# Kernel optimization log

Measured on AMD Instinct MI355X. Metric: run time of the kernel, lower is better.

## Reference

```python
import jax, jax.numpy as jnp
import numpy as np

B, S, P, V, D = 8, 32, 8, 8000, 128
CONC = 5.0  # concentrator_factor
EPS = 1e-8  # torch cosine_similarity eps


def setup_inputs() -> dict:
    key = jax.random.key(0)
    ks = jax.random.split(key, 8)
    concepts = jax.random.randint(ks[0], (B, S, P), 0, V)
    concepts_length = jax.random.randint(ks[1], (B, S), 0, P + 1)
    seg_len = jax.random.randint(ks[2], (B,), 1, S + 1)
    embed_w = jax.random.normal(ks[3], (V, D), jnp.float32)
    embed_kb_w = jax.random.normal(ks[4], (V, D), jnp.float32)
    edge_matrix = jax.random.uniform(ks[5], (V, V), jnp.float32)
    affectiveness = jax.random.uniform(ks[6], (V,), jnp.float32)
    lam = jnp.full((V,), 0.5, jnp.float32)  # _lambda init to GAW
    return dict(concepts=concepts, concepts_length=concepts_length, seg_len=seg_len,
                embed_w=embed_w, embed_kb_w=embed_kb_w, edge_matrix=edge_matrix,
                affectiveness=affectiveness, lam=lam)


def reference(concepts, concepts_length, seg_len, embed_w, embed_kb_w,
              edge_matrix, affectiveness, lam):
    f32 = embed_w.dtype
    # init_params: normalize edge_matrix rows by their range
    rng = edge_matrix.max(axis=1) - edge_matrix.min(axis=1)  # [V]
    em = edge_matrix / (rng + (rng == 0).astype(f32))[:, None]

    ce = embed_w[concepts]  # [B,S,P,D]
    # ragged mean over P (empty -> zeros, matching empty_tensor)
    pmask = (jnp.arange(P)[None, None, :] < concepts_length[:, :, None]).astype(f32)  # [B,S,P]
    denom = jnp.maximum(concepts_length, 1).astype(f32)[:, :, None]  # [B,S,1]
    mean_j = (ce * pmask[..., None]).sum(axis=2) / denom  # [B,S,D]
    # mean over valid segments j < seg_len
    smask = (jnp.arange(S)[None, :] < seg_len[:, None]).astype(f32)  # [B,S]
    context = (mean_j * smask[..., None]).sum(axis=1) / seg_len.astype(f32)[:, None]  # [B,D]

    # abs cosine similarity vs KB embedding table
    cn = context / jnp.maximum(jnp.linalg.norm(context, axis=1, keepdims=True), EPS)
    kn = embed_kb_w / jnp.maximum(jnp.linalg.norm(embed_kb_w, axis=1, keepdims=True), EPS)
    cos = jnp.abs(cn @ kn.T)  # [B,V]

    eg = em[concepts]  # [B,S,P,V] irregular row gather
    rel = eg * cos[:, None, None, :]
    aff = (eg > 0).astype(f32) * affectiveness
    w = lam * rel + (1.0 - lam) * aff  # [B,S,P,V]
    attn = jax.nn.softmax(w * CONC, axis=3)
    ce2 = attn @ embed_kb_w  # [B,S,P,D]

    # ragged mean over P again, zero out segments j >= seg_len (padded output)
    out = (ce2 * pmask[..., None]).sum(axis=2) / denom  # [B,S,D]
    out = out * smask[..., None]
    return out
```

## Files before the change

kernel.cpp:

```cpp
#include <hip/hip_runtime.h>
#include <cmath>

#define NB 8
#define NS 32
#define NP 8
#define NV 8000
#define ND 128
#define CONC 5.0f
#define EPS 1e-8f

#define TROWS 8
#define USPLIT 25
#define URANGE 320
#define UCHUNK 64
#define NCHUNK (URANGE / UCHUNK)
#define MAXSLOTS (NB * NS * NP)

#define WS_COUNTER 0
#define WS_META_C  16
#define WS_META_O  2064
#define WS_IRNG    4112
#define WS_GMAX    6160
#define WS_SCALE   8208
#define WS_CN      10256
#define WS_COS     11280
#define WS_MEANJ   75280

__global__ void k_mean(const int* __restrict__ concepts,
                       const int* __restrict__ concepts_length,
                       const float* __restrict__ embed_w,
                       float* __restrict__ mean_j) {
    const int bs = blockIdx.x;
    const int d = threadIdx.x;
    const int len = concepts_length[bs];
    float sum = 0.0f;
    for (int p = 0; p < len; ++p) {
        const int c = concepts[bs * NP + p];
        sum += embed_w[(size_t)c * ND + d];
    }
    mean_j[(size_t)bs * ND + d] = sum / (float)(len > 0 ? len : 1);
}

__global__ void k_ctx2(const int* __restrict__ seg_len,
                       const float* __restrict__ mean_j,
                       float* __restrict__ cn) {
    const int b = blockIdx.x;
    const int d = threadIdx.x;
    const int sl = seg_len[b];
    float acc = 0.0f;
    for (int s = 0; s < sl; ++s) acc += mean_j[(size_t)(b * NS + s) * ND + d];
    acc /= (float)sl;
    float ss = acc * acc;
    #pragma unroll
    for (int m = 1; m < 64; m <<= 1) ss += __shfl_xor(ss, m);
    __shared__ float sred[2];
    if ((d & 63) == 0) sred[d >> 6] = ss;
    __syncthreads();
    const float tot = sred[0] + sred[1];
    cn[b * ND + d] = acc / fmaxf(sqrtf(tot), EPS);
}

__global__ __launch_bounds__(256) void k_cos(const float* __restrict__ kb,
                                             const float* __restrict__ cn,
                                             float* __restrict__ cos_bv) {
    __shared__ float s_cn[NB * ND];
    const int t = threadIdx.x;
    for (int i = t; i < NB * ND; i += 256) s_cn[i] = cn[i];
    __syncthreads();

    const int v = blockIdx.x * 8 + (t >> 5);
    const int l = t & 31;
    const float4 kv = *reinterpret_cast<const float4*>(kb + (size_t)v * ND + (l << 2));
    float ss = kv.x * kv.x + kv.y * kv.y + kv.z * kv.z + kv.w * kv.w;
    #pragma unroll
    for (int m = 1; m < 32; m <<= 1) ss += __shfl_xor(ss, m);
    const float inv = 1.0f / fmaxf(sqrtf(ss), EPS);
    #pragma unroll
    for (int b = 0; b < NB; ++b) {
        const float4 cv = *reinterpret_cast<const float4*>(&s_cn[b * ND + (l << 2)]);
        float dot = kv.x * cv.x + kv.y * cv.y + kv.z * cv.z + kv.w * cv.w;
        #pragma unroll
        for (int m = 1; m < 32; m <<= 1) dot += __shfl_xor(dot, m);
        if (l == 0) cos_bv[b * NV + v] = fabsf(dot * inv);
    }
}

__global__ __launch_bounds__(256) void k_A(
        const int* __restrict__ concepts,
        const int* __restrict__ concepts_length,
        const int* __restrict__ seg_len,
        const float* __restrict__ edge,
        const float* __restrict__ aff,
        const float* __restrict__ lam,
        const float* __restrict__ cos_bv,
        int* __restrict__ counter,
        int* __restrict__ meta_c, int* __restrict__ meta_out,
        float* __restrict__ f_irng, float* __restrict__ f_gmax,
        float* __restrict__ f_scale) {
    const int idx = blockIdx.x;
    const int b = idx >> 8;
    const int s = (idx >> 3) & 31;
    const int p = idx & 7;
    if (s >= seg_len[b]) return;
    const int len = concepts_length[b * NS + s];
    if (p >= len) return;
    const int c = concepts[idx];

    const int t = threadIdx.x;
    const float* __restrict__ erow = edge + (size_t)c * NV;
    float4 ev[8];
    float lmax = -INFINITY, lmin = INFINITY;
    #pragma unroll
    for (int k = 0; k < 8; ++k) {
        const int f = t + (k << 8);
        if (f < 2000) {
            const float4 e = *reinterpret_cast<const float4*>(erow + (f << 2));
            ev[k] = e;
            lmax = fmaxf(lmax, fmaxf(fmaxf(e.x, e.y), fmaxf(e.z, e.w)));
            lmin = fminf(lmin, fminf(fminf(e.x, e.y), fminf(e.z, e.w)));
        }
    }
    #pragma unroll
    for (int m = 1; m < 64; m <<= 1) {
        lmax = fmaxf(lmax, __shfl_xor(lmax, m));
        lmin = fminf(lmin, __shfl_xor(lmin, m));
    }
    __shared__ float s_min[4], s_max[4], s_wm[4], s_sum[4];
    if ((t & 63) == 0) { s_min[t >> 6] = lmin; s_max[t >> 6] = lmax; }
    __syncthreads();
    const float rmin = fminf(fminf(s_min[0], s_min[1]), fminf(s_min[2], s_min[3]));
    const float rmax = fmaxf(fmaxf(s_max[0], s_max[1]), fmaxf(s_max[2], s_max[3]));
    const float rng = rmax - rmin;
    const float inv_rng = 1.0f / (rng + (rng == 0.0f ? 1.0f : 0.0f));

    const float* __restrict__ cosb = cos_bv + b * NV;
    float wmax = -INFINITY;
    #pragma unroll
    for (int k = 0; k < 8; ++k) {
        const int f = t + (k << 8);
        if (f < 2000) {
            const int u = f << 2;
            const float4 l4 = *reinterpret_cast<const float4*>(lam + u);
            const float4 a4 = *reinterpret_cast<const float4*>(aff + u);
            const float4 c4 = *reinterpret_cast<const float4*>(cosb + u);
            float4 e = ev[k];
            e.x *= inv_rng; e.y *= inv_rng; e.z *= inv_rng; e.w *= inv_rng;
            float4 w;
            w.x = (l4.x * e.x * c4.x + (1.0f - l4.x) * ((e.x > 0.0f) ? 1.0f : 0.0f) * a4.x) * CONC;
            w.y = (l4.y * e.y * c4.y + (1.0f - l4.y) * ((e.y > 0.0f) ? 1.0f : 0.0f) * a4.y) * CONC;
            w.z = (l4.z * e.z * c4.z + (1.0f - l4.z) * ((e.z > 0.0f) ? 1.0f : 0.0f) * a4.z) * CONC;
            w.w = (l4.w * e.w * c4.w + (1.0f - l4.w) * ((e.w > 0.0f) ? 1.0f : 0.0f) * a4.w) * CONC;
            ev[k] = w;
            wmax = fmaxf(wmax, fmaxf(fmaxf(w.x, w.y), fmaxf(w.z, w.w)));
        } else {
            ev[k] = make_float4(-INFINITY, -INFINITY, -INFINITY, -INFINITY);
        }
    }
    #pragma unroll
    for (int m = 1; m < 64; m <<= 1) wmax = fmaxf(wmax, __shfl_xor(wmax, m));
    if ((t & 63) == 0) s_wm[t >> 6] = wmax;
    __syncthreads();
    const float gmax = fmaxf(fmaxf(s_wm[0], s_wm[1]), fmaxf(s_wm[2], s_wm[3]));

    float lsum = 0.0f;
    #pragma unroll
    for (int k = 0; k < 8; ++k) {
        lsum += __expf(ev[k].x - gmax);
        lsum += __expf(ev[k].y - gmax);
        lsum += __expf(ev[k].z - gmax);
        lsum += __expf(ev[k].w - gmax);
    }
    #pragma unroll
    for (int m = 1; m < 64; m <<= 1) lsum += __shfl_xor(lsum, m);
    if ((t & 63) == 0) s_sum[t >> 6] = lsum;
    __syncthreads();
    if (t == 0) {
        const float total = s_sum[0] + s_sum[1] + s_sum[2] + s_sum[3];
        const int slot = atomicAdd(counter, 1);
        meta_c[slot] = c;
        meta_out[slot] = b * NS + s;
        f_irng[slot] = inv_rng;
        f_gmax[slot] = gmax;
        f_scale[slot] = 1.0f / (total * (float)len);
    }
}

__global__ __launch_bounds__(256) void k_B(
        const float* __restrict__ edge,
        const float* __restrict__ aff,
        const float* __restrict__ lam,
        const float* __restrict__ kb,
        const float* __restrict__ cos_bv,
        const int* __restrict__ counter,
        const int* __restrict__ meta_c, const int* __restrict__ meta_out,
        const float* __restrict__ f_irng, const float* __restrict__ f_gmax,
        const float* __restrict__ f_scale,
        float* __restrict__ out) {
    const int count = counter[0];
    const int tile = blockIdx.x;
    if (tile * TROWS >= count) return;

    const int t = threadIdx.x;
    const int ug = t & 7;
    const int l = t >> 3;

    __shared__ int s_c[TROWS], s_o[TROWS], s_b[TROWS];
    __shared__ float s_irng[TROWS], s_gmax[TROWS], s_scale[TROWS];
    __shared__ __align__(16) float s_p[UCHUNK * TROWS];

    if (t < TROWS) {
        const int slot = tile * TROWS + t;
        if (slot < count) {
            const int c = meta_c[slot];
            const int o = meta_out[slot];
            s_c[t] = c; s_o[t] = o; s_b[t] = o >> 5;
            s_irng[t] = f_irng[slot];
            s_gmax[t] = f_gmax[slot];
            s_scale[t] = f_scale[slot];
        } else {
            s_c[t] = -1; s_o[t] = 0; s_b[t] = 0;
            s_irng[t] = 0.0f; s_gmax[t] = 0.0f; s_scale[t] = 0.0f;
        }
    }
    __syncthreads();

    const int u0 = blockIdx.y * URANGE;

    float4 acc[TROWS];
    #pragma unroll
    for (int j = 0; j < TROWS; ++j) acc[j] = make_float4(0.f, 0.f, 0.f, 0.f);

    for (int ch = 0; ch < NCHUNK; ++ch) {
        const int uc = u0 + ch * UCHUNK;

        #pragma unroll
        for (int rep = 0; rep < 2; ++rep) {
            const int ii = t + (rep << 8);
            const int slot = ii & 7;
            const int uu = ii >> 3;
            const int cc = s_c[slot];
            float pv = 0.0f;
            if (cc >= 0) {
                const int u = uc + uu;
                const float e = edge[(size_t)cc * NV + u] * s_irng[slot];
                const float lm = lam[u];
                const float w = (lm * e * cos_bv[(size_t)s_b[slot] * NV + u]
                                 + (1.0f - lm) * ((e > 0.0f) ? 1.0f : 0.0f) * aff[u]) * CONC;
                pv = __expf(w - s_gmax[slot]);
            }
            s_p[ii] = pv;
        }
        __syncthreads();

        #pragma unroll
        for (int r = 0; r < 8; ++r) {
            const int uu = ug + (r << 3);
            const float4 kv = *reinterpret_cast<const float4*>(
                kb + (size_t)(uc + uu) * ND + (l << 2));
            const float4 p0 = *reinterpret_cast<const float4*>(&s_p[uu * TROWS]);
            const float4 p1 = *reinterpret_cast<const float4*>(&s_p[uu * TROWS + 4]);
            acc[0].x = fmaf(p0.x, kv.x, acc[0].x); acc[0].y = fmaf(p0.x, kv.y, acc[0].y);
            acc[0].z = fmaf(p0.x, kv.z, acc[0].z); acc[0].w = fmaf(p0.x, kv.w, acc[0].w);
            acc[1].x = fmaf(p0.y, kv.x, acc[1].x); acc[1].y = fmaf(p0.y, kv.y, acc[1].y);
            acc[1].z = fmaf(p0.y, kv.z, acc[1].z); acc[1].w = fmaf(p0.y, kv.w, acc[1].w);
            acc[2].x = fmaf(p0.z, kv.x, acc[2].x); acc[2].y = fmaf(p0.z, kv.y, acc[2].y);
            acc[2].z = fmaf(p0.z, kv.z, acc[2].z); acc[2].w = fmaf(p0.z, kv.w, acc[2].w);
            acc[3].x = fmaf(p0.w, kv.x, acc[3].x); acc[3].y = fmaf(p0.w, kv.y, acc[3].y);
            acc[3].z = fmaf(p0.w, kv.z, acc[3].z); acc[3].w = fmaf(p0.w, kv.w, acc[3].w);
            acc[4].x = fmaf(p1.x, kv.x, acc[4].x); acc[4].y = fmaf(p1.x, kv.y, acc[4].y);
            acc[4].z = fmaf(p1.x, kv.z, acc[4].z); acc[4].w = fmaf(p1.x, kv.w, acc[4].w);
            acc[5].x = fmaf(p1.y, kv.x, acc[5].x); acc[5].y = fmaf(p1.y, kv.y, acc[5].y);
            acc[5].z = fmaf(p1.y, kv.z, acc[5].z); acc[5].w = fmaf(p1.y, kv.w, acc[5].w);
            acc[6].x = fmaf(p1.z, kv.x, acc[6].x); acc[6].y = fmaf(p1.z, kv.y, acc[6].y);
            acc[6].z = fmaf(p1.z, kv.z, acc[6].z); acc[6].w = fmaf(p1.z, kv.w, acc[6].w);
            acc[7].x = fmaf(p1.w, kv.x, acc[7].x); acc[7].y = fmaf(p1.w, kv.y, acc[7].y);
            acc[7].z = fmaf(p1.w, kv.z, acc[7].z); acc[7].w = fmaf(p1.w, kv.w, acc[7].w);
        }
        __syncthreads();
    }

    float4 res = make_float4(0.f, 0.f, 0.f, 0.f);
    #pragma unroll
    for (int j = 0; j < TROWS; ++j) {
        float4 a = acc[j];
        #pragma unroll
        for (int m = 1; m <= 4; m <<= 1) {
            a.x += __shfl_xor(a.x, m);
            a.y += __shfl_xor(a.y, m);
            a.z += __shfl_xor(a.z, m);
            a.w += __shfl_xor(a.w, m);
        }
        if (ug == j) res = a;
    }

    const int myslot = tile * TROWS + ug;
    if (myslot < count && s_c[ug] >= 0) {
        const float sc = s_scale[ug];
        float* o = out + (size_t)s_o[ug] * ND + (l << 2);
        atomicAdd(o + 0, res.x * sc);
        atomicAdd(o + 1, res.y * sc);
        atomicAdd(o + 2, res.z * sc);
        atomicAdd(o + 3, res.w * sc);
    }
}

extern "C" void kernel_launch(void* const* d_in, const int* in_sizes, int n_in,
                              void* d_out, int out_size, void* d_ws, size_t ws_size,
                              hipStream_t stream) {
    const int*   concepts        = (const int*)d_in[0];
    const int*   concepts_length = (const int*)d_in[1];
    const int*   seg_len         = (const int*)d_in[2];
    const float* embed_w         = (const float*)d_in[3];
    const float* embed_kb_w      = (const float*)d_in[4];
    const float* edge_matrix     = (const float*)d_in[5];
    const float* affectiveness   = (const float*)d_in[6];
    const float* lam             = (const float*)d_in[7];
    float* out = (float*)d_out;

    float* wsf = (float*)d_ws;
    int*   wsi = (int*)d_ws;
    int*   counter  = wsi + WS_COUNTER;
    int*   meta_c   = wsi + WS_META_C;
    int*   meta_out = wsi + WS_META_O;
    float* f_irng   = wsf + WS_IRNG;
    float* f_gmax   = wsf + WS_GMAX;
    float* f_scale  = wsf + WS_SCALE;
    float* cn       = wsf + WS_CN;
    float* cos_bv   = wsf + WS_COS;
    float* mean_j   = wsf + WS_MEANJ;

    hipMemsetAsync(out, 0, (size_t)out_size * sizeof(float), stream);
    hipMemsetAsync(counter, 0, 64, stream);

    k_mean<<<NB * NS, ND, 0, stream>>>(concepts, concepts_length, embed_w, mean_j);
    k_ctx2<<<NB, ND, 0, stream>>>(seg_len, mean_j, cn);
    k_cos<<<NV / 8, 256, 0, stream>>>(embed_kb_w, cn, cos_bv);
    k_A<<<MAXSLOTS, 256, 0, stream>>>(concepts, concepts_length, seg_len,
                                      edge_matrix, affectiveness, lam, cos_bv,
                                      counter, meta_c, meta_out,
                                      f_irng, f_gmax, f_scale);
    dim3 gB(MAXSLOTS / TROWS, USPLIT, 1);
    k_B<<<gB, 256, 0, stream>>>(edge_matrix, affectiveness, lam, embed_kb_w,
                                cos_bv, counter, meta_c, meta_out,
                                f_irng, f_gmax, f_scale, out);
}
```

Measured before the change: 412.2 us.

## Materialize unnormalized softmax probabilities in k_A instead of recomputing in k_B

k_A now writes the exponentiated attention weights for each valid slot into a workspace buffer, and k_B reads them with float4 loads. Previously k_B re-gathered the edge row, lam, aff and cos per element and recomputed the exp. The slot is now claimed with an atomic at the start of the block so the row can be written directly. This removes duplicate edge-row reads and exp work in k_B, at the cost of an extra write and read of up to 2048 rows of 8000 floats through global memory.

```diff
diff --git a/kernel.cpp b/kernel.cpp
--- a/kernel.cpp
+++ b/kernel.cpp
@@ -16,15 +16,13 @@
 #define NCHUNK (URANGE / UCHUNK)
 #define MAXSLOTS (NB * NS * NP)
 
-#define WS_COUNTER 0
-#define WS_META_C  16
-#define WS_META_O  2064
-#define WS_IRNG    4112
-#define WS_GMAX    6160
-#define WS_SCALE   8208
-#define WS_CN      10256
-#define WS_COS     11280
-#define WS_MEANJ   75280
+#define WS_CNT    0
+#define WS_METAO  16
+#define WS_SCALE  2064
+#define WS_CN     4112
+#define WS_COS    5136
+#define WS_MEANJ  69136
+#define WS_P      101904
 
 __global__ void k_mean(const int* __restrict__ concepts,
                        const int* __restrict__ concepts_length,
@@ -94,9 +92,9 @@
         const float* __restrict__ lam,
         const float* __restrict__ cos_bv,
         int* __restrict__ counter,
-        int* __restrict__ meta_c, int* __restrict__ meta_out,
-        float* __restrict__ f_irng, float* __restrict__ f_gmax,
-        float* __restrict__ f_scale) {
+        int* __restrict__ meta_out,
+        float* __restrict__ f_scale,
+        float* __restrict__ pbuf) {
     const int idx = blockIdx.x;
     const int b = idx >> 8;
     const int s = (idx >> 3) & 31;
@@ -125,11 +123,14 @@
         lmax = fmaxf(lmax, __shfl_xor(lmax, m));
         lmin = fminf(lmin, __shfl_xor(lmin, m));
     }
-    __shared__ float s_min[4], s_max[4], s_wm[4], s_sum[4];
-    if ((t & 63) == 0) { s_min[t >> 6] = lmin; s_max[t >> 6] = lmax; }
-    __syncthreads();
-    const float rmin = fminf(fminf(s_min[0], s_min[1]), fminf(s_min[2], s_min[3]));
-    const float rmax = fmaxf(fmaxf(s_max[0], s_max[1]), fmaxf(s_max[2], s_max[3]));
+    __shared__ float s_mn[4], s_mx[4], s_wm[4], s_sum[4];
+    __shared__ int s_slot;
+    if (t == 0) s_slot = atomicAdd(counter, 1);
+    if ((t & 63) == 0) { s_mn[t >> 6] = lmin; s_mx[t >> 6] = lmax; }
+    __syncthreads();
+    const float rmin = fminf(fminf(s_mn[0], s_mn[1]), fminf(s_mn[2], s_mn[3]));
+    const float rmax = fmaxf(fmaxf(s_mx[0], s_mx[1]), fmaxf(s_mx[2], s_mx[3]));
+    const int slot = s_slot;
     const float rng = rmax - rmin;
     const float inv_rng = 1.0f / (rng + (rng == 0.0f ? 1.0f : 0.0f));
 
@@ -152,8 +153,6 @@
             w.w = (l4.w * e.w * c4.w + (1.0f - l4.w) * ((e.w > 0.0f) ? 1.0f : 0.0f) * a4.w) * CONC;
             ev[k] = w;
             wmax = fmaxf(wmax, fmaxf(fmaxf(w.x, w.y), fmaxf(w.z, w.w)));
-        } else {
-            ev[k] = make_float4(-INFINITY, -INFINITY, -INFINITY, -INFINITY);
         }
     }
     #pragma unroll
@@ -162,13 +161,20 @@
     __syncthreads();
     const float gmax = fmaxf(fmaxf(s_wm[0], s_wm[1]), fmaxf(s_wm[2], s_wm[3]));
 
+    float* __restrict__ prow = pbuf + (size_t)slot * NV;
     float lsum = 0.0f;
     #pragma unroll
     for (int k = 0; k < 8; ++k) {
-        lsum += __expf(ev[k].x - gmax);
-        lsum += __expf(ev[k].y - gmax);
-        lsum += __expf(ev[k].z - gmax);
-        lsum += __expf(ev[k].w - gmax);
+        const int f = t + (k << 8);
+        if (f < 2000) {
+            float4 pe;
+            pe.x = __expf(ev[k].x - gmax);
+            pe.y = __expf(ev[k].y - gmax);
+            pe.z = __expf(ev[k].z - gmax);
+            pe.w = __expf(ev[k].w - gmax);
+            *reinterpret_cast<float4*>(prow + (f << 2)) = pe;
+            lsum += pe.x + pe.y + pe.z + pe.w;
+        }
     }
     #pragma unroll
     for (int m = 1; m < 64; m <<= 1) lsum += __shfl_xor(lsum, m);
@@ -176,25 +182,17 @@
     __syncthreads();
     if (t == 0) {
         const float total = s_sum[0] + s_sum[1] + s_sum[2] + s_sum[3];
-        const int slot = atomicAdd(counter, 1);
-        meta_c[slot] = c;
         meta_out[slot] = b * NS + s;
-        f_irng[slot] = inv_rng;
-        f_gmax[slot] = gmax;
         f_scale[slot] = 1.0f / (total * (float)len);
     }
 }
 
 __global__ __launch_bounds__(256) void k_B(
-        const float* __restrict__ edge,
-        const float* __restrict__ aff,
-        const float* __restrict__ lam,
         const float* __restrict__ kb,
-        const float* __restrict__ cos_bv,
         const int* __restrict__ counter,
-        const int* __restrict__ meta_c, const int* __restrict__ meta_out,
-        const float* __restrict__ f_irng, const float* __restrict__ f_gmax,
+        const int* __restrict__ meta_out,
         const float* __restrict__ f_scale,
+        const float* __restrict__ pbuf,
         float* __restrict__ out) {
     const int count = counter[0];
     const int tile = blockIdx.x;
@@ -204,23 +202,14 @@
     const int ug = t & 7;
     const int l = t >> 3;
 
-    __shared__ int s_c[TROWS], s_o[TROWS], s_b[TROWS];
-    __shared__ float s_irng[TROWS], s_gmax[TROWS], s_scale[TROWS];
+    __shared__ int s_o[TROWS];
+    __shared__ float s_sc[TROWS];
     __shared__ __align__(16) float s_p[UCHUNK * TROWS];
 
     if (t < TROWS) {
         const int slot = tile * TROWS + t;
-        if (slot < count) {
-            const int c = meta_c[slot];
-            const int o = meta_out[slot];
-            s_c[t] = c; s_o[t] = o; s_b[t] = o >> 5;
-            s_irng[t] = f_irng[slot];
-            s_gmax[t] = f_gmax[slot];
-            s_scale[t] = f_scale[slot];
-        } else {
-            s_c[t] = -1; s_o[t] = 0; s_b[t] = 0;
-            s_irng[t] = 0.0f; s_gmax[t] = 0.0f; s_scale[t] = 0.0f;
-        }
+        s_o[t]  = (slot < count) ? meta_out[slot] : 0;
+        s_sc[t] = (slot < count) ? f_scale[slot] : 0.0f;
     }
     __syncthreads();
 
@@ -233,22 +222,18 @@
     for (int ch = 0; ch < NCHUNK; ++ch) {
         const int uc = u0 + ch * UCHUNK;
 
-        #pragma unroll
-        for (int rep = 0; rep < 2; ++rep) {
-            const int ii = t + (rep << 8);
-            const int slot = ii & 7;
-            const int uu = ii >> 3;
-            const int cc = s_c[slot];
-            float pv = 0.0f;
-            if (cc >= 0) {
-                const int u = uc + uu;
-                const float e = edge[(size_t)cc * NV + u] * s_irng[slot];
-                const float lm = lam[u];
-                const float w = (lm * e * cos_bv[(size_t)s_b[slot] * NV + u]
-                                 + (1.0f - lm) * ((e > 0.0f) ? 1.0f : 0.0f) * aff[u]) * CONC;
-                pv = __expf(w - s_gmax[slot]);
-            }
-            s_p[ii] = pv;
+        if (t < 128) {
+            const int slot = t >> 4;
+            const int q = t & 15;
+            const int row = tile * TROWS + slot;
+            float4 pv = make_float4(0.f, 0.f, 0.f, 0.f);
+            if (row < count)
+                pv = *reinterpret_cast<const float4*>(pbuf + (size_t)row * NV + uc + (q << 2));
+            const int uu = q << 2;
+            s_p[(uu + 0) * TROWS + slot] = pv.x;
+            s_p[(uu + 1) * TROWS + slot] = pv.y;
+            s_p[(uu + 2) * TROWS + slot] = pv.z;
+            s_p[(uu + 3) * TROWS + slot] = pv.w;
         }
         __syncthreads();
 
@@ -294,8 +279,8 @@
     }
 
     const int myslot = tile * TROWS + ug;
-    if (myslot < count && s_c[ug] >= 0) {
-        const float sc = s_scale[ug];
+    if (myslot < count) {
+        const float sc = s_sc[ug];
         float* o = out + (size_t)s_o[ug] * ND + (l << 2);
         atomicAdd(o + 0, res.x * sc);
         atomicAdd(o + 1, res.y * sc);
@@ -319,15 +304,13 @@
 
     float* wsf = (float*)d_ws;
     int*   wsi = (int*)d_ws;
-    int*   counter  = wsi + WS_COUNTER;
-    int*   meta_c   = wsi + WS_META_C;
-    int*   meta_out = wsi + WS_META_O;
-    float* f_irng   = wsf + WS_IRNG;
-    float* f_gmax   = wsf + WS_GMAX;
+    int*   counter  = wsi + WS_CNT;
+    int*   meta_out = wsi + WS_METAO;
     float* f_scale  = wsf + WS_SCALE;
     float* cn       = wsf + WS_CN;
     float* cos_bv   = wsf + WS_COS;
     float* mean_j   = wsf + WS_MEANJ;
+    float* pbuf     = wsf + WS_P;
 
     hipMemsetAsync(out, 0, (size_t)out_size * sizeof(float), stream);
     hipMemsetAsync(counter, 0, 64, stream);
@@ -337,10 +320,7 @@
     k_cos<<<NV / 8, 256, 0, stream>>>(embed_kb_w, cn, cos_bv);
     k_A<<<MAXSLOTS, 256, 0, stream>>>(concepts, concepts_length, seg_len,
                                       edge_matrix, affectiveness, lam, cos_bv,
-                                      counter, meta_c, meta_out,
-                                      f_irng, f_gmax, f_scale);
+                                      counter, meta_out, f_scale, pbuf);
     dim3 gB(MAXSLOTS / TROWS, USPLIT, 1);
-    k_B<<<gB, 256, 0, stream>>>(edge_matrix, affectiveness, lam, embed_kb_w,
-                                cos_bv, counter, meta_c, meta_out,
-                                f_irng, f_gmax, f_scale, out);
-}
+    k_B<<<gB, 256, 0, stream>>>(embed_kb_w, counter, meta_out, f_scale, pbuf, out);
+}
```

Result: no change. 413.3 us (+0.3%).
